# Kernel optimization log

Measured on AMD Instinct MI355X. Metric: run time of the kernel, lower is better.

Reference implementation:

```python
import jax, jax.numpy as jnp
import numpy as np

Z_DIM = 3
H = 128
N_BLOCKS = 4
N = 30000
E = 180000
T = 2


def _mlp2(x, W1, b1, W2, b2):
    return jnp.maximum(x @ W1 + b1, 0.0) @ W2 + b2


def _stats(x, eps=1e-8):
    # batch mean/std as accumulated by the running-stat Normalizer (buffers -> no grad)
    m = x.mean(0)
    v = jnp.maximum((x * x).mean(0) - m * m, 0.0)
    s = jnp.maximum(jnp.sqrt(v), eps)
    return jax.lax.stop_gradient(m), jax.lax.stop_gradient(s)


def setup_inputs() -> dict:
    key = jax.random.key(0)
    ks = jax.random.split(key, 32)

    def w(k, shape, fan_in):
        return jax.random.normal(k, shape, jnp.float32) / np.sqrt(fan_in).astype(np.float32)

    inp = {}
    inp["z"] = jax.random.normal(ks[0], (T, N, Z_DIM), jnp.float32)
    inp["z_target"] = jax.random.normal(ks[1], (N, Z_DIM), jnp.float32)
    inp["pos"] = jax.random.uniform(ks[2], (N, 2), jnp.float32)
    # encoder node MLP: z_dim -> H -> H
    inp["enc_node_W1"] = w(ks[3], (Z_DIM, H), Z_DIM)
    inp["enc_node_b1"] = jnp.zeros((H,), jnp.float32)
    inp["enc_node_W2"] = w(ks[4], (H, H), H)
    inp["enc_node_b2"] = jnp.zeros((H,), jnp.float32)
    # encoder edge MLP: edge_dim(3) -> H -> H
    inp["enc_edge_W1"] = w(ks[5], (3, H), 3)
    inp["enc_edge_b1"] = jnp.zeros((H,), jnp.float32)
    inp["enc_edge_W2"] = w(ks[6], (H, H), H)
    inp["enc_edge_b2"] = jnp.zeros((H,), jnp.float32)
    # decoder MLP: H -> H -> z_dim
    inp["dec_W1"] = w(ks[7], (H, H), H)
    inp["dec_b1"] = jnp.zeros((H,), jnp.float32)
    inp["dec_W2"] = w(ks[8], (H, Z_DIM), H)
    inp["dec_b2"] = jnp.zeros((Z_DIM,), jnp.float32)
    # GraphNetBlocks, stacked over n_blocks
    inp["blk_edge_W1"] = w(ks[9], (N_BLOCKS, 3 * H, H), 3 * H)
    inp["blk_edge_b1"] = jnp.zeros((N_BLOCKS, H), jnp.float32)
    inp["blk_edge_W2"] = w(ks[10], (N_BLOCKS, H, H), H)
    inp["blk_edge_b2"] = jnp.zeros((N_BLOCKS, H), jnp.float32)
    inp["blk_node_W1"] = w(ks[11], (N_BLOCKS, 2 * H, H), 2 * H)
    inp["blk_node_b1"] = jnp.zeros((N_BLOCKS, H), jnp.float32)
    inp["blk_node_W2"] = w(ks[12], (N_BLOCKS, H, H), H)
    inp["blk_node_b2"] = jnp.zeros((N_BLOCKS, H), jnp.float32)
    # bidirectional mesh edges (triangles_to_edges output)
    inp["senders"] = jax.random.randint(ks[13], (E,), 0, N, jnp.int64)
    inp["receivers"] = jax.random.randint(ks[14], (E,), 0, N, jnp.int64)
    return inp


def reference(z, z_target, pos,
              enc_node_W1, enc_node_b1, enc_node_W2, enc_node_b2,
              enc_edge_W1, enc_edge_b1, enc_edge_W2, enc_edge_b2,
              dec_W1, dec_b1, dec_W2, dec_b2,
              blk_edge_W1, blk_edge_b1, blk_edge_W2, blk_edge_b2,
              blk_node_W1, blk_node_b1, blk_node_W2, blk_node_b2,
              senders, receivers):
    zl = z[-1]                                   # [N, z_dim]
    n_nodes = zl.shape[0]

    # --- build_graph ---
    rel = pos[senders] - pos[receivers]          # [E, 2]
    ef_raw = jnp.concatenate([rel, jnp.linalg.norm(rel, axis=1, keepdims=True)], axis=1)  # [E, 3]
    em, es = _stats(ef_raw)
    ef = _mlp2((ef_raw - em) / es, enc_edge_W1, enc_edge_b1, enc_edge_W2, enc_edge_b2)    # [E, H]
    nm, ns = _stats(zl)
    nf = _mlp2((zl - nm) / ns, enc_node_W1, enc_node_b1, enc_node_W2, enc_node_b2)        # [N, H]

    # --- message passing blocks ---
    def block(carry, p):
        nf, ef = carry
        eW1, eb1, eW2, eb2, nW1, nb1, nW2, nb2 = p
        e_in = jnp.concatenate([ef, nf[senders], nf[receivers]], axis=1)   # [E, 3H]
        ef = _mlp2(e_in, eW1, eb1, eW2, eb2) + ef
        agg = jax.ops.segment_sum(ef, receivers, num_segments=n_nodes)    # [N, H]
        n_in = jnp.concatenate([nf, agg], axis=1)                          # [N, 2H]
        nf = _mlp2(n_in, nW1, nb1, nW2, nb2) + nf
        return (nf, ef), None

    (nf, ef), _ = jax.lax.scan(block, (nf, ef),
                               (blk_edge_W1, blk_edge_b1, blk_edge_W2, blk_edge_b2,
                                blk_node_W1, blk_node_b1, blk_node_W2, blk_node_b2))

    # --- decode + loss ---
    output = _mlp2(nf, dec_W1, dec_b1, dec_W2, dec_b2)                     # [N, z_dim]
    target = z_target - zl
    om, os = _stats(target)
    target_normalized = (target - om) / os
    loss = jnp.mean((target_normalized - output) ** 2)

    z_update = jax.lax.stop_gradient(output) * os + om                     # Normalizer.inverse(detach)
    z_pred = zl + z_update
    rmse = jnp.mean(jnp.sqrt(jnp.mean((z_pred - z_target) ** 2, axis=0)))
    return z_pred, loss, rmse
```

## Files before the change

kernel.cpp:

```cpp
#include <hip/hip_runtime.h>
#include <hip/hip_bf16.h>
#include <math.h>

#define HDIM 128
#define TPB 256

typedef __attribute__((ext_vector_type(8))) short bf16x8;
typedef __attribute__((ext_vector_type(4))) float f32x4;

static inline int ceil_div(int a, int b){ return (a + b - 1) / b; }

__device__ __forceinline__ float wave_sum(float v){
#pragma unroll
  for (int o = 32; o > 0; o >>= 1) v += __shfl_down(v, o, 64);
  return v;
}
__device__ __forceinline__ int wave_sum_i(int v){
#pragma unroll
  for (int o = 32; o > 0; o >>= 1) v += __shfl_down(v, o, 64);
  return v;
}

__device__ __forceinline__ short f2bf(float f){
  __hip_bfloat16 h = __float2bfloat16(f);
  return *reinterpret_cast<short*>(&h);
}
__device__ __forceinline__ float bfb2f(short s){
  unsigned int u = ((unsigned int)(unsigned short)s) << 16;
  return __builtin_bit_cast(float, u);
}

__device__ __forceinline__ void gl_lds16(const short* g, short* l){
  __builtin_amdgcn_global_load_lds(
      (const __attribute__((address_space(1))) void*)g,
      (__attribute__((address_space(3))) void*)l, 16, 0, 0);
}

__global__ void csr_hist(const int* __restrict__ rcv, int* __restrict__ deg, int E){
  int e = blockIdx.x * blockDim.x + threadIdx.x;
  if (e < E) atomicAdd(&deg[rcv[e]], 1);
}

__global__ void scan_pass1(const int* __restrict__ deg, int* __restrict__ bsum, int N){
  __shared__ int red[4];
  int tid = threadIdx.x;
  int base = blockIdx.x * 1024;
  int s = 0;
  for (int i = tid; i < 1024; i += 256){
    int idx = base + i;
    if (idx < N) s += deg[idx];
  }
  s = wave_sum_i(s);
  if ((tid & 63) == 0) red[tid >> 6] = s;
  __syncthreads();
  if (tid == 0) bsum[blockIdx.x] = red[0] + red[1] + red[2] + red[3];
}

__global__ void scan_pass2(const int* __restrict__ bsum, int* __restrict__ boff,
                           int nb, int* __restrict__ row_start, int N, int E){
  if (threadIdx.x == 0){
    int acc = 0;
    for (int b = 0; b < nb; b++){ boff[b] = acc; acc += bsum[b]; }
    row_start[N] = E;
  }
}

__global__ void scan_pass3(const int* __restrict__ deg, const int* __restrict__ boff,
                           int* __restrict__ row_start, int* __restrict__ cursor, int N){
  __shared__ int tsum[256];
  int tid = threadIdx.x;
  int base = blockIdx.x * 1024;
  int i0 = base + tid * 4;
  int v[4];
  int s = 0;
#pragma unroll
  for (int k = 0; k < 4; k++){
    int idx = i0 + k;
    v[k] = (idx < N) ? deg[idx] : 0;
    s += v[k];
  }
  tsum[tid] = s;
  __syncthreads();
  for (int off = 1; off < 256; off <<= 1){
    int val = (tid >= off) ? tsum[tid - off] : 0;
    __syncthreads();
    tsum[tid] += val;
    __syncthreads();
  }
  int excl = (tid == 0) ? 0 : tsum[tid - 1];
  int b = boff[blockIdx.x] + excl;
#pragma unroll
  for (int k = 0; k < 4; k++){
    int idx = i0 + k;
    if (idx < N){
      row_start[idx] = b;
      cursor[idx]    = b;
      b += v[k];
    }
  }
}

__global__ void edge_prep(const float* __restrict__ pos,
                          const int* __restrict__ snd,
                          const int* __restrict__ rcv,
                          int* __restrict__ cursor,
                          int* __restrict__ psnd,
                          int* __restrict__ prcv,
                          float* __restrict__ ef_raw,
                          float* __restrict__ epart, int E){
  __shared__ float red[4][6];
  int tid = threadIdx.x, w = tid >> 6, l = tid & 63;
  int e = blockIdx.x * blockDim.x + tid;
  float s[6] = {0.f,0.f,0.f,0.f,0.f,0.f};
  if (e < E){
    int si = snd[e], ri = rcv[e];
    int p = atomicAdd(&cursor[ri], 1);
    psnd[p] = si;
    prcv[p] = ri;
    float rx = pos[2*si]   - pos[2*ri];
    float ry = pos[2*si+1] - pos[2*ri+1];
    float nm = sqrtf(rx*rx + ry*ry);
    ef_raw[3*p]   = rx;
    ef_raw[3*p+1] = ry;
    ef_raw[3*p+2] = nm;
    s[0] = rx; s[1] = ry; s[2] = nm;
    s[3] = rx*rx; s[4] = ry*ry; s[5] = nm*nm;
  }
#pragma unroll
  for (int k = 0; k < 6; k++) s[k] = wave_sum(s[k]);
  if (l == 0)
#pragma unroll
    for (int k = 0; k < 6; k++) red[w][k] = s[k];
  __syncthreads();
  if (tid < 6)
    epart[(size_t)blockIdx.x * 6 + tid] =
      red[0][tid] + red[1][tid] + red[2][tid] + red[3][tid];
}

__global__ void node_stats(const float* __restrict__ zl,
                           const float* __restrict__ z_target,
                           float* __restrict__ npart, int N){
  __shared__ float red[4][12];
  int tid = threadIdx.x, w = tid >> 6, l = tid & 63;
  int n = blockIdx.x * blockDim.x + tid;
  float s[12];
#pragma unroll
  for (int i = 0; i < 12; i++) s[i] = 0.f;
  if (n < N){
#pragma unroll
    for (int d = 0; d < 3; d++){
      float z = zl[3*n+d];
      float t = z_target[3*n+d] - z;
      s[d]   = z;  s[3+d] = z*z;
      s[6+d] = t;  s[9+d] = t*t;
    }
  }
#pragma unroll
  for (int i = 0; i < 12; i++) s[i] = wave_sum(s[i]);
  if (l == 0)
#pragma unroll
    for (int i = 0; i < 12; i++) red[w][i] = s[i];
  __syncthreads();
  if (tid < 12)
    npart[(size_t)blockIdx.x * 12 + tid] =
      red[0][tid] + red[1][tid] + red[2][tid] + red[3][tid];
}

__global__ void reduce_finalize(const float* __restrict__ ep, int ne,
                                const float* __restrict__ np_, int nn,
                                float* __restrict__ fin, int E, int N){
  __shared__ float red[4];
  __shared__ float raw[18];
  int tid = threadIdx.x, w = tid >> 6, l = tid & 63;
  for (int j = 0; j < 6; j++){
    float s = 0.f;
    for (int b = tid; b < ne; b += 256) s += ep[(size_t)b * 6 + j];
    s = wave_sum(s);
    if (l == 0) red[w] = s;
    __syncthreads();
    if (tid == 0) raw[j] = red[0] + red[1] + red[2] + red[3];
    __syncthreads();
  }
  for (int j = 0; j < 12; j++){
    float s = 0.f;
    for (int b = tid; b < nn; b += 256) s += np_[(size_t)b * 12 + j];
    s = wave_sum(s);
    if (l == 0) red[w] = s;
    __syncthreads();
    if (tid == 0) raw[6 + j] = red[0] + red[1] + red[2] + red[3];
    __syncthreads();
  }
  if (tid == 0){
#pragma unroll
    for (int d = 0; d < 3; d++){
      float cE = (float)E, cN = (float)N;
      float m, v;
      m = raw[0+d] / cE; v = fmaxf(raw[3+d]/cE - m*m, 0.f);
      fin[0+d] = m;  fin[3+d]  = fmaxf(sqrtf(v), 1e-8f);
      m = raw[6+d] / cN; v = fmaxf(raw[9+d]/cN - m*m, 0.f);
      fin[6+d] = m;  fin[9+d]  = fmaxf(sqrtf(v), 1e-8f);
      m = raw[12+d] / cN; v = fmaxf(raw[15+d]/cN - m*m, 0.f);
      fin[12+d] = m; fin[15+d] = fmaxf(sqrtf(v), 1e-8f);
    }
  }
}

__global__ void pack_weights(const float* __restrict__ encEW2,
                             const float* __restrict__ encNW2,
                             const float* __restrict__ decW1,
                             const float* __restrict__ beW1,
                             const float* __restrict__ beW2,
                             const float* __restrict__ bnW1,
                             const float* __restrict__ bnW2,
                             __hip_bfloat16* __restrict__ wp){
  int y = blockIdx.y;
  const float* src; __hip_bfloat16* dst; int K;
  if (y == 0){ src = encEW2; dst = wp;          K = 128; }
  else if (y == 1){ src = encNW2; dst = wp + 16384; K = 128; }
  else if (y == 2){ src = decW1;  dst = wp + 32768; K = 128; }
  else {
    int b = (y - 3) >> 2, j = (y - 3) & 3;
    __hip_bfloat16* base = wp + 49152 + b * 114688;
    if (j == 0){ src = beW1 + b*49152; dst = base;          K = 384; }
    else if (j == 1){ src = beW2 + b*16384; dst = base + 49152; K = 128; }
    else if (j == 2){ src = bnW1 + b*32768; dst = base + 65536; K = 256; }
    else { src = bnW2 + b*16384; dst = base + 98304; K = 128; }
  }
  int id = blockIdx.x * blockDim.x + threadIdx.x;
  if (id >= 128 * K) return;
  int c = id >> 12;
  int r = id & 4095;
  int t = r >> 9;
  int l = (r >> 3) & 63;
  int j = r & 7;
  int k = c * 32 + ((l >> 4) << 3) + j;
  int n = t * 16 + (l & 15);
  dst[id] = __float2bfloat16(src[k * 128 + n]);
}

__launch_bounds__(256)
__global__ void encoder_fused(const float* __restrict__ raw,
                              const float* __restrict__ mptr,
                              const float* __restrict__ sptr,
                              const float* __restrict__ W1,
                              const float* __restrict__ b1,
                              const __hip_bfloat16* __restrict__ W2f,
                              const float* __restrict__ b2,
                              __hip_bfloat16* __restrict__ out, int rows){
  __shared__ __align__(16) short bsh[16384];
  const int tid = threadIdx.x, w = tid >> 6, l = tid & 63, m = l & 15, q = l >> 4;
  const short* wsrc = (const short*)W2f;
#pragma unroll
  for (int i = 0; i < 8; i++){
    int inst = w * 8 + i;
    gl_lds16(wsrc + inst * 512 + l * 8, &bsh[inst * 512]);
  }
  float s0 = mptr[0], s1 = mptr[1], s2 = mptr[2];
  float d0 = sptr[0], d1 = sptr[1], d2 = sptr[2];
  const int row0 = blockIdx.x * 64 + w * 16;
  const int ra = min(row0 + m, rows - 1);
  float x0 = (raw[3*ra]   - s0) / d0;
  float x1 = (raw[3*ra+1] - s1) / d1;
  float x2 = (raw[3*ra+2] - s2) / d2;
  bf16x8 afr[4];
#pragma unroll
  for (int c = 0; c < 4; c++){
    int nb = c * 32 + q * 8;
#pragma unroll
    for (int j = 0; j < 8; j++){
      float h = b1[nb+j] + x0 * W1[nb+j] + x1 * W1[128+nb+j] + x2 * W1[256+nb+j];
      afr[c][j] = f2bf(fmaxf(h, 0.f));
    }
  }
  f32x4 acc[8];
#pragma unroll
  for (int t = 0; t < 8; t++) acc[t] = (f32x4){0.f,0.f,0.f,0.f};
  __syncthreads();
#pragma unroll
  for (int c = 0; c < 4; c++){
#pragma unroll
    for (int t = 0; t < 8; t++){
      bf16x8 b = *(const bf16x8*)&bsh[(c*8 + t)*512 + l*8];
      acc[t] = __builtin_amdgcn_mfma_f32_16x16x32_bf16(afr[c], b, acc[t], 0, 0, 0);
    }
  }
  const int row_d = row0 + q * 4;
#pragma unroll
  for (int t = 0; t < 8; t++){
    int col = t * 16 + m;
    float bb = b2[col];
#pragma unroll
    for (int r = 0; r < 4; r++){
      int e = row_d + r;
      if (e < rows) out[(size_t)e * HDIM + col] = __float2bfloat16(acc[t][r] + bb);
    }
  }
}

__launch_bounds__(256)
__global__ void gemm128_g(const __hip_bfloat16* __restrict__ A,
                          const __hip_bfloat16* __restrict__ Wf,
                          const float* __restrict__ bias,
                          float* __restrict__ out, int rows){
  __shared__ __align__(16) short bsh[16384];
  const int tid = threadIdx.x, w = tid >> 6, l = tid & 63, m = l & 15, q = l >> 4;
  const short* wsrc = (const short*)Wf;
#pragma unroll
  for (int i = 0; i < 8; i++){
    int inst = w * 8 + i;
    gl_lds16(wsrc + inst * 512 + l * 8, &bsh[inst * 512]);
  }
  const int row0 = blockIdx.x * 64 + w * 16;
  const int ra = min(row0 + m, rows - 1);
  const short* pa = (const short*)A + (size_t)ra * HDIM + q * 8;
  bf16x8 afr[4];
#pragma unroll
  for (int c = 0; c < 4; c++) afr[c] = *(const bf16x8*)(pa + c * 32);
  f32x4 acc[8];
#pragma unroll
  for (int t = 0; t < 8; t++) acc[t] = (f32x4){0.f,0.f,0.f,0.f};
  __syncthreads();
#pragma unroll
  for (int c = 0; c < 4; c++){
#pragma unroll
    for (int t = 0; t < 8; t++){
      bf16x8 b = *(const bf16x8*)&bsh[(c*8 + t)*512 + l*8];
      acc[t] = __builtin_amdgcn_mfma_f32_16x16x32_bf16(afr[c], b, acc[t], 0, 0, 0);
    }
  }
  const int row_d = row0 + q * 4;
#pragma unroll
  for (int t = 0; t < 8; t++){
    int col = t * 16 + m;
    float bb = bias[col];
#pragma unroll
    for (int r = 0; r < 4; r++){
      int e = row_d + r;
      if (e < rows) out[(size_t)e * HDIM + col] = fmaxf(acc[t][r] + bb, 0.f);
    }
  }
}

__launch_bounds__(512)
__global__ void msg_pre(const __hip_bfloat16* __restrict__ nf,
                        const __hip_bfloat16* __restrict__ eWf,
                        __hip_bfloat16* __restrict__ u, int N){
  __shared__ __align__(16) short wsh[32768];
  const int tid = threadIdx.x, w = tid >> 6, l = tid & 63, m = l & 15, q = l >> 4;
  const short* wsrc = (const short*)eWf + 4 * 4096;
#pragma unroll
  for (int i = 0; i < 8; i++){
    int inst = w * 8 + i;
    gl_lds16(wsrc + inst * 512 + l * 8, &wsh[inst * 512]);
  }
  const int row0 = blockIdx.x * 128 + w * 16;
  const int ra = min(row0 + m, N - 1);
  const short* pa = (const short*)nf + (size_t)ra * HDIM + q * 8;
  bf16x8 afr[4];
#pragma unroll
  for (int c = 0; c < 4; c++) afr[c] = *(const bf16x8*)(pa + c * 32);
  f32x4 acc[16];
#pragma unroll
  for (int t = 0; t < 16; t++) acc[t] = (f32x4){0.f,0.f,0.f,0.f};
  __syncthreads();
#pragma unroll
  for (int c = 0; c < 4; c++){
#pragma unroll
    for (int t = 0; t < 16; t++){
      int cc = (t < 8) ? c : (4 + c);
      bf16x8 b = *(const bf16x8*)&wsh[cc * 4096 + (t & 7) * 512 + l * 8];
      acc[t] = __builtin_amdgcn_mfma_f32_16x16x32_bf16(afr[c], b, acc[t], 0, 0, 0);
    }
  }
  const int row_d = row0 + q * 4;
#pragma unroll
  for (int t = 0; t < 16; t++){
    int col = t * 16 + m;
#pragma unroll
    for (int r = 0; r < 4; r++){
      int n = row_d + r;
      if (n < N) u[(size_t)n * 256 + col] = __float2bfloat16(acc[t][r]);
    }
  }
}

__launch_bounds__(512)
__global__ void edge_block(const int* __restrict__ psnd,
                           const int* __restrict__ prcv,
                           const __hip_bfloat16* __restrict__ u,
                           __hip_bfloat16* __restrict__ ef,
                           const __hip_bfloat16* __restrict__ Wfrag,
                           const float* __restrict__ b1,
                           const float* __restrict__ b2,
                           int E){
  __shared__ __align__(16) short bsh[2][4096];
  __shared__ __align__(16) short hsh[8][16][136];
  const int tid = threadIdx.x, w = tid >> 6, l = tid & 63, m = l & 15, q = l >> 4;
  const short* wsrc = (const short*)Wfrag;
  gl_lds16(wsrc + w*512 + l*8, &bsh[0][w*512]);

  const int row0 = blockIdx.x * 128 + w * 16;
  const int ra = min(row0 + m, E - 1);
  const short* pe = (const short*)ef + (size_t)ra * HDIM + q * 8;
  bf16x8 afr[4];
#pragma unroll
  for (int c = 0; c < 4; c++) afr[c] = *(const bf16x8*)(pe + c * 32);

  {
    int grow = min(row0 + (l >> 2), E - 1);
    int us_row = psnd[grow], ur_row = prcv[grow];
    const short* pus = (const short*)u + (size_t)us_row * 256 + (l & 3) * 32;
    const short* pur = (const short*)u + (size_t)ur_row * 256 + 128 + (l & 3) * 32;
    short* hdst = &hsh[w][l >> 2][(l & 3) * 32];
#pragma unroll
    for (int k = 0; k < 4; k++){
      bf16x8 a = *(const bf16x8*)(pus + k * 8);
      bf16x8 b = *(const bf16x8*)(pur + k * 8);
      bf16x8 s;
#pragma unroll
      for (int j = 0; j < 8; j++) s[j] = f2bf(bfb2f(a[j]) + bfb2f(b[j]));
      *(bf16x8*)(hdst + k * 8) = s;
    }
  }
  const int orow = row0 + (l >> 2);
  const int orc = min(orow, E - 1);
  const short* pold = (const short*)ef + (size_t)orc * HDIM + (l & 3) * 32;
  bf16x8 vold[4];
#pragma unroll
  for (int k = 0; k < 4; k++) vold[k] = *(const bf16x8*)(pold + k * 8);

  f32x4 acc[8];
#pragma unroll
  for (int t = 0; t < 8; t++) acc[t] = (f32x4){0.f,0.f,0.f,0.f};
  __syncthreads();
#pragma unroll
  for (int c = 0; c < 4; c++){
    if (c + 1 < 4)
      gl_lds16(wsrc + (c+1)*4096 + w*512 + l*8, &bsh[(c+1)&1][w*512]);
    const short* bb = &bsh[c & 1][0];
#pragma unroll
    for (int t = 0; t < 8; t++){
      bf16x8 b = *(const bf16x8*)(bb + t*512 + l*8);
      acc[t] = __builtin_amdgcn_mfma_f32_16x16x32_bf16(afr[c], b, acc[t], 0, 0, 0);
    }
    if (c + 1 < 4) __syncthreads();
  }
#pragma unroll
  for (int t = 0; t < 8; t++){
    float bb = b1[t * 16 + m];
#pragma unroll
    for (int r = 0; r < 4; r++){
      float uval = bfb2f(hsh[w][q*4 + r][t*16 + m]);
      hsh[w][q*4 + r][t*16 + m] = f2bf(fmaxf(acc[t][r] + uval + bb, 0.f));
    }
  }
  const short* ph = &hsh[w][m][0] + q * 8;
  const short* w2 = wsrc + 49152;
  f32x4 acc2[8];
#pragma unroll
  for (int t = 0; t < 8; t++) acc2[t] = (f32x4){0.f,0.f,0.f,0.f};
#pragma unroll
  for (int c = 0; c < 4; c++){
    bf16x8 a = *(const bf16x8*)(ph + c * 32);
#pragma unroll
    for (int t = 0; t < 8; t++){
      bf16x8 b = *(const bf16x8*)(w2 + ((c*8 + t)*64 + l)*8);
      acc2[t] = __builtin_amdgcn_mfma_f32_16x16x32_bf16(a, b, acc2[t], 0, 0, 0);
    }
  }
#pragma unroll
  for (int t = 0; t < 8; t++){
    float bb = b2[t * 16 + m];
#pragma unroll
    for (int r = 0; r < 4; r++)
      hsh[w][q*4 + r][t*16 + m] = f2bf(acc2[t][r] + bb);
  }
  if (orow < E){
    const short* src = &hsh[w][l >> 2][(l & 3) * 32];
    short* dst = (short*)ef + (size_t)orow * HDIM + (l & 3) * 32;
#pragma unroll
    for (int k = 0; k < 4; k++){
      bf16x8 vnew = *(const bf16x8*)(src + k * 8);
      bf16x8 vo;
#pragma unroll
      for (int j = 0; j < 8; j++) vo[j] = f2bf(bfb2f(vnew[j]) + bfb2f(vold[k][j]));
      *(bf16x8*)(dst + k * 8) = vo;
    }
  }
}

__launch_bounds__(512)
__global__ void node_block(const int* __restrict__ row_start,
                           const __hip_bfloat16* __restrict__ ef,
                           __hip_bfloat16* __restrict__ nf,
                           const __hip_bfloat16* __restrict__ Wfrag,
                           const float* __restrict__ b1,
                           const float* __restrict__ b2,
                           int N){
  __shared__ __align__(16) short bsh[2][4096];
  __shared__ __align__(16) short hsh[8][16][136];
  const int tid = threadIdx.x, w = tid >> 6, l = tid & 63, m = l & 15, q = l >> 4;
  const short* wsrc = (const short*)Wfrag;
  gl_lds16(wsrc + w*512 + l*8, &bsh[0][w*512]);

  const int row0 = blockIdx.x * 128 + w * 16;
  const int ra = min(row0 + m, N - 1);
  const short* pn = (const short*)nf + (size_t)ra * HDIM + q * 8;
  bf16x8 afr[8];
#pragma unroll
  for (int c = 0; c < 4; c++) afr[c] = *(const bf16x8*)(pn + c * 32);
  const int orow = row0 + (l >> 2);
  const int orc = min(orow, N - 1);
  const short* pold = (const short*)nf + (size_t)orc * HDIM + (l & 3) * 32;
  bf16x8 vold[4];
#pragma unroll
  for (int k = 0; k < 4; k++) vold[k] = *(const bf16x8*)(pold + k * 8);

  float sum[4][8];
#pragma unroll
  for (int c = 0; c < 4; c++)
#pragma unroll
    for (int j = 0; j < 8; j++) sum[c][j] = 0.f;
  int s0 = row_start[ra], s1 = row_start[ra + 1];
  for (int it = s0; it < s1; it++){
    const short* pf = (const short*)ef + (size_t)it * HDIM + q * 8;
#pragma unroll
    for (int c = 0; c < 4; c++){
      bf16x8 v = *(const bf16x8*)(pf + c * 32);
#pragma unroll
      for (int j = 0; j < 8; j++) sum[c][j] += bfb2f(v[j]);
    }
  }
#pragma unroll
  for (int c = 0; c < 4; c++)
#pragma unroll
    for (int j = 0; j < 8; j++) afr[4 + c][j] = f2bf(sum[c][j]);

  f32x4 acc[8];
#pragma unroll
  for (int t = 0; t < 8; t++) acc[t] = (f32x4){0.f,0.f,0.f,0.f};
  __syncthreads();
#pragma unroll
  for (int c = 0; c < 8; c++){
    if (c + 1 < 8)
      gl_lds16(wsrc + (c+1)*4096 + w*512 + l*8, &bsh[(c+1)&1][w*512]);
    const short* bb = &bsh[c & 1][0];
#pragma unroll
    for (int t = 0; t < 8; t++){
      bf16x8 b = *(const bf16x8*)(bb + t*512 + l*8);
      acc[t] = __builtin_amdgcn_mfma_f32_16x16x32_bf16(afr[c], b, acc[t], 0, 0, 0);
    }
    if (c + 1 < 8) __syncthreads();
  }
#pragma unroll
  for (int t = 0; t < 8; t++){
    float bb = b1[t * 16 + m];
#pragma unroll
    for (int r = 0; r < 4; r++)
      hsh[w][q*4 + r][t*16 + m] = f2bf(fmaxf(acc[t][r] + bb, 0.f));
  }
  const short* ph = &hsh[w][m][0] + q * 8;
  const short* w2 = wsrc + 32768;
  f32x4 acc2[8];
#pragma unroll
  for (int t = 0; t < 8; t++) acc2[t] = (f32x4){0.f,0.f,0.f,0.f};
#pragma unroll
  for (int c = 0; c < 4; c++){
    bf16x8 a = *(const bf16x8*)(ph + c * 32);
#pragma unroll
    for (int t = 0; t < 8; t++){
      bf16x8 b = *(const bf16x8*)(w2 + ((c*8 + t)*64 + l)*8);
      acc2[t] = __builtin_amdgcn_mfma_f32_16x16x32_bf16(a, b, acc2[t], 0, 0, 0);
    }
  }
#pragma unroll
  for (int t = 0; t < 8; t++){
    float bb = b2[t * 16 + m];
#pragma unroll
    for (int r = 0; r < 4; r++)
      hsh[w][q*4 + r][t*16 + m] = f2bf(acc2[t][r] + bb);
  }
  if (orow < N){
    const short* src = &hsh[w][l >> 2][(l & 3) * 32];
    short* dst = (short*)nf + (size_t)orow * HDIM + (l & 3) * 32;
#pragma unroll
    for (int k = 0; k < 4; k++){
      bf16x8 vnew = *(const bf16x8*)(src + k * 8);
      bf16x8 vo;
#pragma unroll
      for (int j = 0; j < 8; j++) vo[j] = f2bf(bfb2f(vnew[j]) + bfb2f(vold[k][j]));
      *(bf16x8*)(dst + k * 8) = vo;
    }
  }
}

__global__ void dec_final(const float* __restrict__ hbuf,
                          const float* __restrict__ W2,
                          const float* __restrict__ b2,
                          float* __restrict__ outd, int rows){
  __shared__ float hl[64 * 129];
  __shared__ float Wl[HDIM * 3];
  __shared__ float bl[3];
  int t = threadIdx.x;
  int node0 = blockIdx.x * 64;
  for (int i = t; i < HDIM * 3; i += 256) Wl[i] = W2[i];
  if (t < 3) bl[t] = b2[t];
#pragma unroll
  for (int i = 0; i < 32; i++){
    int lin = t + i * 256;
    int r = lin >> 7;
    int c = lin & 127;
    int node = node0 + r;
    hl[r * 129 + c] = (node < rows) ? hbuf[(size_t)node * HDIM + c] : 0.f;
  }
  __syncthreads();
  if (t < 64){
    int node = node0 + t;
    if (node < rows){
      float a0 = bl[0], a1 = bl[1], a2 = bl[2];
      for (int k = 0; k < HDIM; k++){
        float v = hl[t * 129 + k];
        a0 += v * Wl[k * 3];
        a1 += v * Wl[k * 3 + 1];
        a2 += v * Wl[k * 3 + 2];
      }
      outd[3 * node]     = a0;
      outd[3 * node + 1] = a1;
      outd[3 * node + 2] = a2;
    }
  }
}

__global__ void epilogue(const float* __restrict__ dec_out,
                         const float* __restrict__ zl,
                         const float* __restrict__ z_target,
                         const float* __restrict__ fin,
                         float* __restrict__ d_out,
                         float* __restrict__ lpart, int N){
  __shared__ float red[4][4];
  int tid = threadIdx.x, w = tid >> 6, l = tid & 63;
  int n = blockIdx.x * blockDim.x + tid;
  float s[4] = {0.f,0.f,0.f,0.f};
  if (n < N){
#pragma unroll
    for (int d = 0; d < 3; d++){
      float om = fin[12 + d], os = fin[15 + d];
      float o   = dec_out[3*n + d];
      float zld = zl[3*n + d];
      float zt  = z_target[3*n + d];
      float tgt = zt - zld;
      float tn  = (tgt - om) / os;
      float diff = tn - o;
      s[0] += diff * diff;
      float zp = zld + o * os + om;
      d_out[3*n + d] = zp;
      float e = zp - zt;
      s[1 + d] = e * e;
    }
  }
#pragma unroll
  for (int k = 0; k < 4; k++) s[k] = wave_sum(s[k]);
  if (l == 0)
#pragma unroll
    for (int k = 0; k < 4; k++) red[w][k] = s[k];
  __syncthreads();
  if (tid < 4)
    lpart[(size_t)blockIdx.x * 4 + tid] =
      red[0][tid] + red[1][tid] + red[2][tid] + red[3][tid];
}

__global__ void finalize_out(const float* __restrict__ lpart, int nb,
                             float* __restrict__ d_out, int N){
  __shared__ float red[4];
  __shared__ float vals[4];
  int tid = threadIdx.x, w = tid >> 6, l = tid & 63;
  for (int j = 0; j < 4; j++){
    float s = 0.f;
    for (int b = tid; b < nb; b += 256) s += lpart[(size_t)b * 4 + j];
    s = wave_sum(s);
    if (l == 0) red[w] = s;
    __syncthreads();
    if (tid == 0) vals[j] = red[0] + red[1] + red[2] + red[3];
    __syncthreads();
  }
  if (tid == 0){
    float cN = (float)N;
    float loss = vals[0] / (3.f * cN);
    float rmse = (sqrtf(vals[1] / cN) + sqrtf(vals[2] / cN) + sqrtf(vals[3] / cN)) / 3.f;
    d_out[(size_t)3 * N]     = loss;
    d_out[(size_t)3 * N + 1] = rmse;
  }
}

extern "C" void kernel_launch(void* const* d_in, const int* in_sizes, int n_in,
                              void* d_out, int out_size, void* d_ws, size_t ws_size,
                              hipStream_t stream){
  const float* z           = (const float*)d_in[0];
  const float* z_target    = (const float*)d_in[1];
  const float* pos         = (const float*)d_in[2];
  const float* enc_node_W1 = (const float*)d_in[3];
  const float* enc_node_b1 = (const float*)d_in[4];
  const float* enc_node_W2 = (const float*)d_in[5];
  const float* enc_node_b2 = (const float*)d_in[6];
  const float* enc_edge_W1 = (const float*)d_in[7];
  const float* enc_edge_b1 = (const float*)d_in[8];
  const float* enc_edge_W2 = (const float*)d_in[9];
  const float* enc_edge_b2 = (const float*)d_in[10];
  const float* dec_W1      = (const float*)d_in[11];
  const float* dec_b1      = (const float*)d_in[12];
  const float* dec_W2      = (const float*)d_in[13];
  const float* dec_b2      = (const float*)d_in[14];
  const float* blk_edge_W1 = (const float*)d_in[15];
  const float* blk_edge_b1 = (const float*)d_in[16];
  const float* blk_edge_W2 = (const float*)d_in[17];
  const float* blk_edge_b2 = (const float*)d_in[18];
  const float* blk_node_W1 = (const float*)d_in[19];
  const float* blk_node_b1 = (const float*)d_in[20];
  const float* blk_node_W2 = (const float*)d_in[21];
  const float* blk_node_b2 = (const float*)d_in[22];
  const int*   senders     = (const int*)d_in[23];
  const int*   receivers   = (const int*)d_in[24];

  const int N = in_sizes[1] / 3;
  const int E = in_sizes[23];
  const float* zl = z + (size_t)N * 3;

  const int neb = ceil_div(E, TPB);
  const int nnb = ceil_div(N, TPB);
  const int nsb = ceil_div(N, 1024);

  char* p = (char*)d_ws;
  auto carve = [&](size_t bytes) -> char* {
    char* r = p; p += (bytes + 255) & ~(size_t)255; return r;
  };
  float* stats_fin = (float*)carve(32 * 4);
  float* epart     = (float*)carve((size_t)neb * 6 * 4);
  float* npart     = (float*)carve((size_t)nnb * 12 * 4);
  float* lpart     = (float*)carve((size_t)nnb * 4 * 4);
  float* ef_raw    = (float*)carve((size_t)E * 3 * 4);
  float* dec_out   = (float*)carve((size_t)N * 3 * 4);
  float* hbuf      = (float*)carve((size_t)N * HDIM * 4);
  int*   deg       = (int*)carve((size_t)N * 4);
  int*   bsum      = (int*)carve((size_t)(nsb + 1) * 4);
  int*   boff      = (int*)carve((size_t)(nsb + 1) * 4);
  int*   row_start = (int*)carve((size_t)(N + 1) * 4);
  int*   cursor    = (int*)carve((size_t)N * 4);
  int*   psnd      = (int*)carve((size_t)E * 4);
  int*   prcv      = (int*)carve((size_t)E * 4);
  __hip_bfloat16* wp = (__hip_bfloat16*)carve((size_t)507904 * 2);
  __hip_bfloat16* ef = (__hip_bfloat16*)carve((size_t)E * HDIM * 2);
  __hip_bfloat16* nf = (__hip_bfloat16*)carve((size_t)N * HDIM * 2);
  __hip_bfloat16* u  = (__hip_bfloat16*)carve((size_t)N * 256 * 2);

  float* out = (float*)d_out;

  hipMemsetAsync(deg, 0, (size_t)N * 4, stream);

  csr_hist<<<neb, TPB, 0, stream>>>(receivers, deg, E);
  scan_pass1<<<nsb, TPB, 0, stream>>>(deg, bsum, N);
  scan_pass2<<<1, 64, 0, stream>>>(bsum, boff, nsb, row_start, N, E);
  scan_pass3<<<nsb, TPB, 0, stream>>>(deg, boff, row_start, cursor, N);
  edge_prep<<<neb, TPB, 0, stream>>>(pos, senders, receivers, cursor,
                                     psnd, prcv, ef_raw, epart, E);

  node_stats<<<nnb, TPB, 0, stream>>>(zl, z_target, npart, N);
  reduce_finalize<<<1, TPB, 0, stream>>>(epart, neb, npart, nnb, stats_fin, E, N);

  pack_weights<<<dim3(192, 19), TPB, 0, stream>>>(enc_edge_W2, enc_node_W2, dec_W1,
                                                  blk_edge_W1, blk_edge_W2,
                                                  blk_node_W1, blk_node_W2, wp);

  encoder_fused<<<ceil_div(E, 64), TPB, 0, stream>>>(ef_raw, stats_fin + 0, stats_fin + 3,
                                                     enc_edge_W1, enc_edge_b1,
                                                     wp, enc_edge_b2, ef, E);
  encoder_fused<<<ceil_div(N, 64), TPB, 0, stream>>>(zl, stats_fin + 6, stats_fin + 9,
                                                     enc_node_W1, enc_node_b1,
                                                     wp + 16384, enc_node_b2, nf, N);

  for (int b = 0; b < 4; b++){
    const __hip_bfloat16* eWf = wp + 49152 + (size_t)b * 114688;
    const __hip_bfloat16* nWf = eWf + 65536;
    const float* eb1 = blk_edge_b1 + (size_t)b * 128;
    const float* eb2 = blk_edge_b2 + (size_t)b * 128;
    const float* nb1 = blk_node_b1 + (size_t)b * 128;
    const float* nb2 = blk_node_b2 + (size_t)b * 128;

    msg_pre<<<ceil_div(N, 128), 512, 0, stream>>>(nf, eWf, u, N);
    edge_block<<<ceil_div(E, 128), 512, 0, stream>>>(psnd, prcv, u, ef,
                                                     eWf, eb1, eb2, E);
    node_block<<<ceil_div(N, 128), 512, 0, stream>>>(row_start, ef, nf,
                                                     nWf, nb1, nb2, N);
  }

  gemm128_g<<<ceil_div(N, 64), TPB, 0, stream>>>(nf, wp + 32768, dec_b1, hbuf, N);
  dec_final<<<ceil_div(N, 64), TPB, 0, stream>>>(hbuf, dec_W2, dec_b2, dec_out, N);

  epilogue<<<nnb, TPB, 0, stream>>>(dec_out, zl, z_target, stats_fin,
                                    out, lpart, N);
  finalize_out<<<1, TPB, 0, stream>>>(lpart, nnb, out, N);
}
```

Baseline: 525.7 us.

## Stage all GEMM weights in LDS and halve node-side block sizes

edge_block now loads the full first-layer weight slab into LDS up front instead of double-buffering chunk by chunk. It then restages the second-layer weights into LDS rather than reading them from global memory inside the MFMA loop. node_block and msg_pre shrink to 256-thread blocks covering 64 rows, which gives more blocks for the small node count, and node_block stages weights in pairs of chunks with fewer barriers. The residual old-value loads move to the epilogue, which lowers register pressure, at the cost of extra barriers and larger LDS footprints that may limit occupancy.

```diff
diff --git a/kernel.cpp b/kernel.cpp
--- a/kernel.cpp
+++ b/kernel.cpp
@@ -341,7 +341,7 @@
   }
 }
 
-__launch_bounds__(512)
+__launch_bounds__(256)
 __global__ void msg_pre(const __hip_bfloat16* __restrict__ nf,
                         const __hip_bfloat16* __restrict__ eWf,
                         __hip_bfloat16* __restrict__ u, int N){
@@ -349,11 +349,11 @@
   const int tid = threadIdx.x, w = tid >> 6, l = tid & 63, m = l & 15, q = l >> 4;
   const short* wsrc = (const short*)eWf + 4 * 4096;
 #pragma unroll
-  for (int i = 0; i < 8; i++){
-    int inst = w * 8 + i;
+  for (int i = 0; i < 16; i++){
+    int inst = i * 4 + w;
     gl_lds16(wsrc + inst * 512 + l * 8, &wsh[inst * 512]);
   }
-  const int row0 = blockIdx.x * 128 + w * 16;
+  const int row0 = blockIdx.x * 64 + w * 16;
   const int ra = min(row0 + m, N - 1);
   const short* pa = (const short*)nf + (size_t)ra * HDIM + q * 8;
   bf16x8 afr[4];
@@ -393,12 +393,15 @@
                            const float* __restrict__ b1,
                            const float* __restrict__ b2,
                            int E){
-  __shared__ __align__(16) short bsh[2][4096];
+  __shared__ __align__(16) short bsh[16384];
   __shared__ __align__(16) short hsh[8][16][136];
   const int tid = threadIdx.x, w = tid >> 6, l = tid & 63, m = l & 15, q = l >> 4;
   const short* wsrc = (const short*)Wfrag;
-  gl_lds16(wsrc + w*512 + l*8, &bsh[0][w*512]);
-
+#pragma unroll
+  for (int i = 0; i < 4; i++){
+    int inst = i * 8 + w;
+    gl_lds16(wsrc + inst * 512 + l * 8, &bsh[inst * 512]);
+  }
   const int row0 = blockIdx.x * 128 + w * 16;
   const int ra = min(row0 + m, E - 1);
   const short* pe = (const short*)ef + (size_t)ra * HDIM + q * 8;
@@ -422,28 +425,23 @@
       *(bf16x8*)(hdst + k * 8) = s;
     }
   }
-  const int orow = row0 + (l >> 2);
-  const int orc = min(orow, E - 1);
-  const short* pold = (const short*)ef + (size_t)orc * HDIM + (l & 3) * 32;
-  bf16x8 vold[4];
-#pragma unroll
-  for (int k = 0; k < 4; k++) vold[k] = *(const bf16x8*)(pold + k * 8);
-
   f32x4 acc[8];
 #pragma unroll
   for (int t = 0; t < 8; t++) acc[t] = (f32x4){0.f,0.f,0.f,0.f};
   __syncthreads();
 #pragma unroll
   for (int c = 0; c < 4; c++){
-    if (c + 1 < 4)
-      gl_lds16(wsrc + (c+1)*4096 + w*512 + l*8, &bsh[(c+1)&1][w*512]);
-    const short* bb = &bsh[c & 1][0];
 #pragma unroll
     for (int t = 0; t < 8; t++){
-      bf16x8 b = *(const bf16x8*)(bb + t*512 + l*8);
+      bf16x8 b = *(const bf16x8*)&bsh[(c*8 + t)*512 + l*8];
       acc[t] = __builtin_amdgcn_mfma_f32_16x16x32_bf16(afr[c], b, acc[t], 0, 0, 0);
     }
-    if (c + 1 < 4) __syncthreads();
+  }
+  __syncthreads();
+#pragma unroll
+  for (int i = 0; i < 4; i++){
+    int inst = i * 8 + w;
+    gl_lds16(wsrc + 49152 + inst * 512 + l * 8, &bsh[inst * 512]);
   }
 #pragma unroll
   for (int t = 0; t < 8; t++){
@@ -454,18 +452,17 @@
       hsh[w][q*4 + r][t*16 + m] = f2bf(fmaxf(acc[t][r] + uval + bb, 0.f));
     }
   }
+  __syncthreads();
   const short* ph = &hsh[w][m][0] + q * 8;
-  const short* w2 = wsrc + 49152;
-  f32x4 acc2[8];
-#pragma unroll
-  for (int t = 0; t < 8; t++) acc2[t] = (f32x4){0.f,0.f,0.f,0.f};
+#pragma unroll
+  for (int t = 0; t < 8; t++) acc[t] = (f32x4){0.f,0.f,0.f,0.f};
 #pragma unroll
   for (int c = 0; c < 4; c++){
     bf16x8 a = *(const bf16x8*)(ph + c * 32);
 #pragma unroll
     for (int t = 0; t < 8; t++){
-      bf16x8 b = *(const bf16x8*)(w2 + ((c*8 + t)*64 + l)*8);
-      acc2[t] = __builtin_amdgcn_mfma_f32_16x16x32_bf16(a, b, acc2[t], 0, 0, 0);
+      bf16x8 b = *(const bf16x8*)&bsh[(c*8 + t)*512 + l*8];
+      acc[t] = __builtin_amdgcn_mfma_f32_16x16x32_bf16(a, b, acc[t], 0, 0, 0);
     }
   }
 #pragma unroll
@@ -473,23 +470,35 @@
     float bb = b2[t * 16 + m];
 #pragma unroll
     for (int r = 0; r < 4; r++)
-      hsh[w][q*4 + r][t*16 + m] = f2bf(acc2[t][r] + bb);
-  }
+      hsh[w][q*4 + r][t*16 + m] = f2bf(acc[t][r] + bb);
+  }
+  const int orow = row0 + (l >> 2);
   if (orow < E){
+    const short* pold = (const short*)ef + (size_t)orow * HDIM + (l & 3) * 32;
     const short* src = &hsh[w][l >> 2][(l & 3) * 32];
     short* dst = (short*)ef + (size_t)orow * HDIM + (l & 3) * 32;
 #pragma unroll
     for (int k = 0; k < 4; k++){
       bf16x8 vnew = *(const bf16x8*)(src + k * 8);
-      bf16x8 vo;
-#pragma unroll
-      for (int j = 0; j < 8; j++) vo[j] = f2bf(bfb2f(vnew[j]) + bfb2f(vold[k][j]));
-      *(bf16x8*)(dst + k * 8) = vo;
-    }
-  }
-}
-
-__launch_bounds__(512)
+      bf16x8 vo   = *(const bf16x8*)(pold + k * 8);
+      bf16x8 vr;
+#pragma unroll
+      for (int j = 0; j < 8; j++) vr[j] = f2bf(bfb2f(vnew[j]) + bfb2f(vo[j]));
+      *(bf16x8*)(dst + k * 8) = vr;
+    }
+  }
+}
+
+#define NB_COMPUTE_CHUNK(c) do {                                               \
+  const short* bb_ = &bsh[(((c) >> 1) & 1) * 8192 + ((c) & 1) * 4096];         \
+  _Pragma("unroll")                                                            \
+  for (int t = 0; t < 8; t++){                                                 \
+    bf16x8 b = *(const bf16x8*)(bb_ + t * 512 + l * 8);                        \
+    acc[t] = __builtin_amdgcn_mfma_f32_16x16x32_bf16(afr[c], b, acc[t], 0, 0, 0); \
+  }                                                                            \
+} while(0)
+
+__launch_bounds__(256)
 __global__ void node_block(const int* __restrict__ row_start,
                            const __hip_bfloat16* __restrict__ ef,
                            __hip_bfloat16* __restrict__ nf,
@@ -497,24 +506,25 @@
                            const float* __restrict__ b1,
                            const float* __restrict__ b2,
                            int N){
-  __shared__ __align__(16) short bsh[2][4096];
-  __shared__ __align__(16) short hsh[8][16][136];
+  __shared__ __align__(16) short bsh[16384];
+  __shared__ __align__(16) short hsh[4][16][136];
   const int tid = threadIdx.x, w = tid >> 6, l = tid & 63, m = l & 15, q = l >> 4;
   const short* wsrc = (const short*)Wfrag;
-  gl_lds16(wsrc + w*512 + l*8, &bsh[0][w*512]);
-
-  const int row0 = blockIdx.x * 128 + w * 16;
+  auto stage_pair = [&](int p){
+    const short* s = wsrc + p * 8192;
+    short* d = &bsh[(p & 1) * 8192];
+#pragma unroll
+    for (int i = 0; i < 4; i++)
+      gl_lds16(s + (i*4 + w)*512 + l*8, d + (i*4 + w)*512);
+  };
+  stage_pair(0); stage_pair(1);
+
+  const int row0 = blockIdx.x * 64 + w * 16;
   const int ra = min(row0 + m, N - 1);
   const short* pn = (const short*)nf + (size_t)ra * HDIM + q * 8;
   bf16x8 afr[8];
 #pragma unroll
   for (int c = 0; c < 4; c++) afr[c] = *(const bf16x8*)(pn + c * 32);
-  const int orow = row0 + (l >> 2);
-  const int orc = min(orow, N - 1);
-  const short* pold = (const short*)nf + (size_t)orc * HDIM + (l & 3) * 32;
-  bf16x8 vold[4];
-#pragma unroll
-  for (int k = 0; k < 4; k++) vold[k] = *(const bf16x8*)(pold + k * 8);
 
   float sum[4][8];
 #pragma unroll
@@ -540,17 +550,25 @@
 #pragma unroll
   for (int t = 0; t < 8; t++) acc[t] = (f32x4){0.f,0.f,0.f,0.f};
   __syncthreads();
-#pragma unroll
-  for (int c = 0; c < 8; c++){
-    if (c + 1 < 8)
-      gl_lds16(wsrc + (c+1)*4096 + w*512 + l*8, &bsh[(c+1)&1][w*512]);
-    const short* bb = &bsh[c & 1][0];
-#pragma unroll
-    for (int t = 0; t < 8; t++){
-      bf16x8 b = *(const bf16x8*)(bb + t*512 + l*8);
-      acc[t] = __builtin_amdgcn_mfma_f32_16x16x32_bf16(afr[c], b, acc[t], 0, 0, 0);
-    }
-    if (c + 1 < 8) __syncthreads();
+  NB_COMPUTE_CHUNK(0);
+  NB_COMPUTE_CHUNK(1);
+  __syncthreads();
+  stage_pair(2);
+  NB_COMPUTE_CHUNK(2);
+  NB_COMPUTE_CHUNK(3);
+  __syncthreads();
+  stage_pair(3);
+  NB_COMPUTE_CHUNK(4);
+  NB_COMPUTE_CHUNK(5);
+  __syncthreads();
+  NB_COMPUTE_CHUNK(6);
+  NB_COMPUTE_CHUNK(7);
+  __syncthreads();
+  {
+    const short* s = wsrc + 32768;
+#pragma unroll
+    for (int i = 0; i < 8; i++)
+      gl_lds16(s + (i*4 + w)*512 + l*8, &bsh[(i*4 + w)*512]);
   }
 #pragma unroll
   for (int t = 0; t < 8; t++){
@@ -559,18 +577,17 @@
     for (int r = 0; r < 4; r++)
       hsh[w][q*4 + r][t*16 + m] = f2bf(fmaxf(acc[t][r] + bb, 0.f));
   }
+  __syncthreads();
   const short* ph = &hsh[w][m][0] + q * 8;
-  const short* w2 = wsrc + 32768;
-  f32x4 acc2[8];
-#pragma unroll
-  for (int t = 0; t < 8; t++) acc2[t] = (f32x4){0.f,0.f,0.f,0.f};
+#pragma unroll
+  for (int t = 0; t < 8; t++) acc[t] = (f32x4){0.f,0.f,0.f,0.f};
 #pragma unroll
   for (int c = 0; c < 4; c++){
     bf16x8 a = *(const bf16x8*)(ph + c * 32);
 #pragma unroll
     for (int t = 0; t < 8; t++){
-      bf16x8 b = *(const bf16x8*)(w2 + ((c*8 + t)*64 + l)*8);
-      acc2[t] = __builtin_amdgcn_mfma_f32_16x16x32_bf16(a, b, acc2[t], 0, 0, 0);
+      bf16x8 b = *(const bf16x8*)&bsh[(c*8 + t)*512 + l*8];
+      acc[t] = __builtin_amdgcn_mfma_f32_16x16x32_bf16(a, b, acc[t], 0, 0, 0);
     }
   }
 #pragma unroll
@@ -578,18 +595,21 @@
     float bb = b2[t * 16 + m];
 #pragma unroll
     for (int r = 0; r < 4; r++)
-      hsh[w][q*4 + r][t*16 + m] = f2bf(acc2[t][r] + bb);
-  }
+      hsh[w][q*4 + r][t*16 + m] = f2bf(acc[t][r] + bb);
+  }
+  const int orow = row0 + (l >> 2);
   if (orow < N){
+    const short* pold = (const short*)nf + (size_t)orow * HDIM + (l & 3) * 32;
     const short* src = &hsh[w][l >> 2][(l & 3) * 32];
     short* dst = (short*)nf + (size_t)orow * HDIM + (l & 3) * 32;
 #pragma unroll
     for (int k = 0; k < 4; k++){
       bf16x8 vnew = *(const bf16x8*)(src + k * 8);
-      bf16x8 vo;
-#pragma unroll
-      for (int j = 0; j < 8; j++) vo[j] = f2bf(bfb2f(vnew[j]) + bfb2f(vold[k][j]));
-      *(bf16x8*)(dst + k * 8) = vo;
+      bf16x8 vo   = *(const bf16x8*)(pold + k * 8);
+      bf16x8 vr;
+#pragma unroll
+      for (int j = 0; j < 8; j++) vr[j] = f2bf(bfb2f(vnew[j]) + bfb2f(vo[j]));
+      *(bf16x8*)(dst + k * 8) = vr;
     }
   }
 }
@@ -785,11 +805,11 @@
     const float* nb1 = blk_node_b1 + (size_t)b * 128;
     const float* nb2 = blk_node_b2 + (size_t)b * 128;
 
-    msg_pre<<<ceil_div(N, 128), 512, 0, stream>>>(nf, eWf, u, N);
+    msg_pre<<<ceil_div(N, 64), 256, 0, stream>>>(nf, eWf, u, N);
     edge_block<<<ceil_div(E, 128), 512, 0, stream>>>(psnd, prcv, u, ef,
                                                      eWf, eb1, eb2, E);
-    node_block<<<ceil_div(N, 128), 512, 0, stream>>>(row_start, ef, nf,
-                                                     nWf, nb1, nb2, N);
+    node_block<<<ceil_div(N, 64), 256, 0, stream>>>(row_start, ef, nf,
+                                                    nWf, nb1, nb2, N);
   }
 
   gemm128_g<<<ceil_div(N, 64), TPB, 0, stream>>>(nf, wp + 32768, dec_b1, hbuf, N);
```

Result: faster. 500.8 us (-4.7%).
